# Optimization experiments

Measured on AMD Instinct MI355X. Metric: run time of the kernel, lower is better.

Reference implementation:

```python
import jax, jax.numpy as jnp
import numpy as np
from jax import lax

B, S, H = 4, 2048, 2048
E, TOPK = 32, 8
I_MOE = 768
I_SHARED = 4096


def setup_inputs() -> dict:
    key = jax.random.key(0)
    ks = jax.random.split(key, 9)
    sc = 0.02
    return {
        "hidden_states": jax.random.normal(ks[0], (B, S, H), jnp.float32),
        "gate_w": jax.random.normal(ks[1], (H, E), jnp.float32) * sc,
        "Wg": jax.random.normal(ks[2], (E, H, I_MOE), jnp.float32) * sc,
        "Wu": jax.random.normal(ks[3], (E, H, I_MOE), jnp.float32) * sc,
        "Wd": jax.random.normal(ks[4], (E, I_MOE, H), jnp.float32) * sc,
        "Sg": jax.random.normal(ks[5], (H, I_SHARED), jnp.float32) * sc,
        "Su": jax.random.normal(ks[6], (H, I_SHARED), jnp.float32) * sc,
        "Sd": jax.random.normal(ks[7], (I_SHARED, H), jnp.float32) * sc,
        "shared_gate_w": jax.random.normal(ks[8], (H, 1), jnp.float32) * sc,
    }


def reference(hidden_states, gate_w, Wg, Wu, Wd, Sg, Su, Sd, shared_gate_w):
    b, s, h = hidden_states.shape
    x = hidden_states.reshape(-1, h)                      # [T, H]
    T = x.shape[0]

    # router: softmax in fp32, top-k, renormalize (norm_topk_prob=True)
    router_logits = x @ gate_w                            # [T, E]
    probs = jax.nn.softmax(router_logits.astype(jnp.float32), axis=-1)
    topk_w, topk_idx = lax.top_k(probs, TOPK)             # [T, K]
    topk_w = topk_w / jnp.sum(topk_w, axis=-1, keepdims=True)
    topk_w = topk_w.astype(x.dtype)

    # dense combine weights: zero for unrouted (token, expert) pairs
    combine = jnp.zeros((T, E), x.dtype).at[jnp.arange(T)[:, None], topk_idx].add(topk_w)

    # scan over experts: SwiGLU MLP, weighted accumulate (scatter-combine)
    def step(acc, packed):
        wg, wu, wd, cw = packed                           # cw: [T]
        hmid = jax.nn.silu(x @ wg) * (x @ wu)             # [T, I_MOE]
        return acc + (hmid @ wd) * cw[:, None], None

    moe_out, _ = lax.scan(step, jnp.zeros_like(x), (Wg, Wu, Wd, combine.T))

    # shared expert with sigmoid gate
    shared = (jax.nn.silu(x @ Sg) * (x @ Su)) @ Sd        # [T, H]
    shared = jax.nn.sigmoid(x @ shared_gate_w) * shared

    final = (moe_out + shared).reshape(b, s, h)
    return final, router_logits
```

## Files before the change

### kernel.cpp

```cpp
#include <hip/hip_runtime.h>
#include <stdint.h>

#define T_TOK 8192
#define HD    2048
#define NE    32
#define KTOP  8
#define IM    768
#define IS    4096

typedef unsigned short u16;
typedef __attribute__((ext_vector_type(8))) short bf16x8;
typedef __attribute__((ext_vector_type(4))) float f32x4;

__device__ __forceinline__ u16 f2b(float f) {
    union { float f; unsigned u; } c; c.f = f;
    unsigned u = c.u;
    return (u16)((u + 0x7FFFu + ((u >> 16) & 1u)) >> 16);
}

__device__ __forceinline__ void gld16(const void* g, void* l) {
    __builtin_amdgcn_global_load_lds(
        (__attribute__((address_space(1))) void*)(uintptr_t)g,
        (__attribute__((address_space(3))) void*)(uint32_t)(uintptr_t)l,
        16, 0, 0);
}

__global__ __launch_bounds__(256) void router_kernel(
    const float* __restrict__ x, const float* __restrict__ gate_w,
    const float* __restrict__ sgw, float* __restrict__ logits_out,
    u16* __restrict__ xb, float* __restrict__ sgvals,
    int* __restrict__ topk_idx, float* __restrict__ topk_w,
    int* __restrict__ counts)
{
    const int t = blockIdx.x, tid = threadIdx.x;
    __shared__ __align__(16) float xrow[HD];
    __shared__ float red[256];
    __shared__ float sh_logit[NE];

    const float4* xr = (const float4*)(x + (size_t)t * HD);
    float4 v0 = xr[tid * 2], v1 = xr[tid * 2 + 1];
    *(float4*)&xrow[tid * 8]     = v0;
    *(float4*)&xrow[tid * 8 + 4] = v1;
    ushort4 p0; p0.x = f2b(v0.x); p0.y = f2b(v0.y); p0.z = f2b(v0.z); p0.w = f2b(v0.w);
    ushort4 p1; p1.x = f2b(v1.x); p1.y = f2b(v1.y); p1.z = f2b(v1.z); p1.w = f2b(v1.w);
    *(ushort4*)&xb[(size_t)t * HD + tid * 8]     = p0;
    *(ushort4*)&xb[(size_t)t * HD + tid * 8 + 4] = p1;
    __syncthreads();

    const int e = tid & 31, seg = tid >> 5;
    float acc = 0.f;
    const float* gwp = gate_w + e;
    for (int j = seg * 256; j < seg * 256 + 256; ++j)
        acc = fmaf(xrow[j], gwp[j * NE], acc);
    red[tid] = acc;
    __syncthreads();
    if (tid < NE) {
        float l = 0.f;
        #pragma unroll
        for (int s = 0; s < 8; ++s) l += red[s * 32 + tid];
        sh_logit[tid] = l;
        logits_out[(size_t)t * NE + tid] = l;
    }
    __syncthreads();

    float sacc = v0.x * sgw[tid * 8 + 0] + v0.y * sgw[tid * 8 + 1] + v0.z * sgw[tid * 8 + 2] + v0.w * sgw[tid * 8 + 3]
               + v1.x * sgw[tid * 8 + 4] + v1.y * sgw[tid * 8 + 5] + v1.z * sgw[tid * 8 + 6] + v1.w * sgw[tid * 8 + 7];
    red[tid] = sacc;
    __syncthreads();
    if (tid < 128) red[tid] += red[tid + 128];
    __syncthreads();
    if (tid < 64) {
        float s2 = red[tid] + red[tid + 64];
        #pragma unroll
        for (int off = 32; off; off >>= 1) s2 += __shfl_xor(s2, off, 64);
        if (tid == 0) sgvals[t] = 1.f / (1.f + __expf(-s2));

        float v = (tid < NE) ? sh_logit[tid] : -3.0e38f;
        float m = v;
        #pragma unroll
        for (int off = 32; off; off >>= 1) m = fmaxf(m, __shfl_xor(m, off, 64));
        float p = __expf(v - m);
        if (tid >= NE) p = 0.f;
        float ssum = p;
        #pragma unroll
        for (int off = 32; off; off >>= 1) ssum += __shfl_xor(ssum, off, 64);
        float myp = p / ssum;

        float selv[KTOP]; int seli[KTOP];
        float sumtop = 0.f;
        #pragma unroll
        for (int k = 0; k < KTOP; ++k) {
            float bv = myp; int bi = tid;
            #pragma unroll
            for (int off = 32; off; off >>= 1) {
                float ov = __shfl_xor(bv, off, 64);
                int   oi = __shfl_xor(bi, off, 64);
                if (ov > bv || (ov == bv && oi < bi)) { bv = ov; bi = oi; }
            }
            selv[k] = bv; seli[k] = bi; sumtop += bv;
            if (tid == bi) myp = -1.f;
        }
        if (tid == 0) {
            #pragma unroll
            for (int k = 0; k < KTOP; ++k) {
                topk_idx[(size_t)t * KTOP + k] = seli[k];
                topk_w[(size_t)t * KTOP + k]   = selv[k] / sumtop;
                atomicAdd(&counts[seli[k]], 1);
            }
        }
    }
}

__global__ void offsets_kernel(const int* __restrict__ counts,
                               int* __restrict__ offsets, int* __restrict__ cursor)
{
    if (threadIdx.x == 0) {
        int a = 0;
        for (int e = 0; e < NE; ++e) { offsets[e] = a; cursor[e] = a; a += counts[e]; }
    }
}

__global__ __launch_bounds__(256) void scatter_kernel(
    const int* __restrict__ topk_idx, const float* __restrict__ topk_w,
    int* __restrict__ cursor, int* __restrict__ token_list, float* __restrict__ weight_list)
{
    int i = blockIdx.x * 256 + threadIdx.x;
    int e = topk_idx[i];
    int pos = atomicAdd(&cursor[e], 1);
    token_list[pos]  = i >> 3;
    weight_list[pos] = topk_w[i];
}

__global__ __launch_bounds__(256) void convert_k(
    const float* __restrict__ W, u16* __restrict__ P, int K, int N)
{
    const int n0 = blockIdx.x * 128, kt = blockIdx.y * 32;
    const size_t eoff = (size_t)blockIdx.z * K * N;
    const int tid = threadIdx.x;
    __shared__ __align__(16) float tile[32][128];

    const float* Wb = W + eoff + (size_t)kt * N + n0;
    #pragma unroll
    for (int p = 0; p < 4; ++p) {
        int k = p * 8 + (tid >> 5);
        *(float4*)&tile[k][(tid & 31) * 4] = *(const float4*)(Wb + (size_t)k * N + (tid & 31) * 4);
    }
    __syncthreads();

    const int kblk = K >> 5;
    u16* Pp = P + eoff + ((size_t)blockIdx.x * kblk + blockIdx.y) * 4096;
    #pragma unroll
    for (int s = 0; s < 2; ++s) {
        int i = s * 256 + tid;
        int c = i >> 7, n = i & 127;
        union { u16 us[8]; uint4 v; } pk;
        #pragma unroll
        for (int q = 0; q < 8; ++q) pk.us[q] = f2b(tile[c * 8 + q][n]);
        *(uint4*)&Pp[(size_t)i * 8] = pk.v;
    }
}

template<int MODE>
__global__ __launch_bounds__(256, 2) void gemm_f(
    const u16* __restrict__ Asrc, const u16* __restrict__ B0p,
    const u16* __restrict__ B1p, u16* __restrict__ outb,
    float* __restrict__ outf, const float* __restrict__ scale,
    const int* __restrict__ token_list, const int* __restrict__ counts,
    const int* __restrict__ offsets)
{
    constexpr bool DUAL   = (MODE == 0 || MODE == 2);
    constexpr bool EXPERT = (MODE >= 2);
    constexpr int KTOT = (MODE == 0 || MODE == 2) ? HD : (MODE == 1 ? IS : IM);
    constexpr int NTOT = (MODE == 0) ? IS : (MODE == 2 ? IM : HD);
    constexpr int NTIL = DUAL ? 3 : 2;
    constexpr int NKT  = KTOT / 32;

    const int tid = threadIdx.x;
    const int ex  = blockIdx.z;
    const int n_e = EXPERT ? counts[ex]  : T_TOK;
    const int off = EXPERT ? offsets[ex] : 0;
    const int m0  = blockIdx.y * 128;
    if (m0 >= n_e) return;
    const int n0 = blockIdx.x * 128;

    const size_t ewoff = EXPERT ? (size_t)ex * KTOT * NTOT : 0;

    __shared__ __align__(16) u16 sh[2 * NTIL * 4096];

    const int w = tid >> 6, lane = tid & 63;
    const int lr = lane & 15, quad = lane >> 4;
    const int wm = (w >> 1) * 64, wn = (w & 1) * 64;
    const int ldsw = w * 512;

    const u16* asrc[2];
    #pragma unroll
    for (int s = 0; s < 2; ++s) {
        int i = s * 256 + tid;
        int c = i >> 7, r = i & 127;
        int grow = m0 + r;
        int gc = grow < n_e ? grow : n_e - 1;
        size_t rowidx;
        if (MODE == 0 || MODE == 1) rowidx = (size_t)grow;
        else if (MODE == 2) rowidx = (size_t)token_list[off + gc];
        else rowidx = (size_t)(off + gc);
        asrc[s] = Asrc + rowidx * KTOT + c * 8;
    }
    const u16* b0 = B0p + ewoff + ((size_t)(n0 >> 7) * NKT) * 4096 + (size_t)tid * 8;
    const u16* b1 = nullptr;
    if constexpr (DUAL) b1 = B1p + ewoff + ((size_t)(n0 >> 7) * NKT) * 4096 + (size_t)tid * 8;

    auto stage = [&](int buf, int kt) {
        u16* A  = sh + (size_t)(buf * NTIL + 0) * 4096;
        u16* Bt = sh + (size_t)(buf * NTIL + 1) * 4096;
        #pragma unroll
        for (int s = 0; s < 2; ++s) {
            gld16(asrc[s] + kt, A + s * 2048 + ldsw);
            gld16(b0 + (size_t)(kt >> 5) * 4096 + s * 2048, Bt + s * 2048 + ldsw);
        }
        if constexpr (DUAL) {
            u16* Bu = sh + (size_t)(buf * NTIL + 2) * 4096;
            #pragma unroll
            for (int s = 0; s < 2; ++s)
                gld16(b1 + (size_t)(kt >> 5) * 4096 + s * 2048, Bu + s * 2048 + ldsw);
        }
    };

    f32x4 acc0[4][4], acc1[4][4];
    #pragma unroll
    for (int a = 0; a < 4; ++a)
        #pragma unroll
        for (int b = 0; b < 4; ++b)
            #pragma unroll
            for (int q = 0; q < 4; ++q) { acc0[a][b][q] = 0.f; if constexpr (DUAL) acc1[a][b][q] = 0.f; }

    stage(0, 0);
    int cur = 0;
    for (int kt = 0; kt < KTOT; kt += 32) {
        __syncthreads();
        if (kt + 32 < KTOT) stage(cur ^ 1, kt + 32);

        const u16* A  = sh + (size_t)(cur * NTIL + 0) * 4096;
        const u16* B0 = sh + (size_t)(cur * NTIL + 1) * 4096;

        bf16x8 af[4], bf0[4], bf1[4];
        #pragma unroll
        for (int mt = 0; mt < 4; ++mt)
            af[mt]  = *(const bf16x8*)&A [quad * 1024 + (wm + mt * 16 + lr) * 8];
        #pragma unroll
        for (int nt = 0; nt < 4; ++nt)
            bf0[nt] = *(const bf16x8*)&B0[quad * 1024 + (wn + nt * 16 + lr) * 8];
        if constexpr (DUAL) {
            const u16* B1 = sh + (size_t)(cur * NTIL + 2) * 4096;
            #pragma unroll
            for (int nt = 0; nt < 4; ++nt)
                bf1[nt] = *(const bf16x8*)&B1[quad * 1024 + (wn + nt * 16 + lr) * 8];
        }
        #pragma unroll
        for (int mt = 0; mt < 4; ++mt)
            #pragma unroll
            for (int nt = 0; nt < 4; ++nt) {
                acc0[mt][nt] = __builtin_amdgcn_mfma_f32_16x16x32_bf16(af[mt], bf0[nt], acc0[mt][nt], 0, 0, 0);
                if constexpr (DUAL)
                    acc1[mt][nt] = __builtin_amdgcn_mfma_f32_16x16x32_bf16(af[mt], bf1[nt], acc1[mt][nt], 0, 0, 0);
            }
        cur ^= 1;
    }

    if (MODE == 0 || MODE == 2) {
        #pragma unroll
        for (int mt = 0; mt < 4; ++mt)
            #pragma unroll
            for (int rg = 0; rg < 4; ++rg) {
                const int grow = m0 + wm + mt * 16 + quad * 4 + rg;
                if (!EXPERT || grow < n_e) {
                    u16* orow = outb + (size_t)(EXPERT ? (off + grow) : grow) * NTOT + n0 + wn + lr;
                    #pragma unroll
                    for (int nt = 0; nt < 4; ++nt) {
                        float g = acc0[mt][nt][rg];
                        float u = acc1[mt][nt][rg];
                        float sgm = 1.f / (1.f + __expf(-g));
                        orow[nt * 16] = f2b(g * sgm * u);
                    }
                }
            }
    } else if (MODE == 1) {
        #pragma unroll
        for (int mt = 0; mt < 4; ++mt)
            #pragma unroll
            for (int rg = 0; rg < 4; ++rg) {
                const int grow = m0 + wm + mt * 16 + quad * 4 + rg;
                const float s = scale[grow];
                float* orow = outf + (size_t)grow * HD + n0 + wn + lr;
                #pragma unroll
                for (int nt = 0; nt < 4; ++nt) orow[nt * 16] = s * acc0[mt][nt][rg];
            }
    } else {
        #pragma unroll
        for (int mt = 0; mt < 4; ++mt)
            #pragma unroll
            for (int rg = 0; rg < 4; ++rg) {
                const int grow = m0 + wm + mt * 16 + quad * 4 + rg;
                if (grow < n_e) {
                    const int tok   = token_list[off + grow];
                    const float wgt = scale[off + grow];
                    float* orow = outf + (size_t)tok * HD + n0 + wn + lr;
                    #pragma unroll
                    for (int nt = 0; nt < 4; ++nt)
                        unsafeAtomicAdd(&orow[nt * 16], wgt * acc0[mt][nt][rg]);
                }
            }
    }
}

template<int MODE>
__global__ __launch_bounds__(256, 2) void gemm_l(
    const u16* __restrict__ Asrc, const float* __restrict__ B0g,
    const float* __restrict__ B1g, u16* __restrict__ outb,
    float* __restrict__ outf, const float* __restrict__ scale,
    const int* __restrict__ token_list, const int* __restrict__ counts,
    const int* __restrict__ offsets)
{
    constexpr bool DUAL   = (MODE == 0 || MODE == 2);
    constexpr bool EXPERT = (MODE >= 2);
    constexpr int KTOT = (MODE == 0 || MODE == 2) ? HD : (MODE == 1 ? IS : IM);
    constexpr int NTOT = (MODE == 0) ? IS : (MODE == 2 ? IM : HD);
    constexpr int LDA  = (MODE == 0 || MODE == 2) ? HD : (MODE == 1 ? IS : IM);

    const int tid = threadIdx.x;
    const int ex  = blockIdx.z;
    const int n_e = EXPERT ? counts[ex]  : T_TOK;
    const int off = EXPERT ? offsets[ex] : 0;
    const int m0  = blockIdx.y * 128;
    if (m0 >= n_e) return;
    const int n0 = blockIdx.x * 128;

    const float* B0 = B0g + (EXPERT ? (size_t)ex * KTOT * NTOT : 0);
    const float* B1 = DUAL ? (B1g + (EXPERT ? (size_t)ex * KTOT * NTOT : 0)) : nullptr;

    __shared__ __align__(16) u16 As [128 * 40];
    __shared__ __align__(16) u16 Bs0[128 * 40];
    __shared__ __align__(16) u16 Bs1[DUAL ? 128 * 40 : 8];

    const u16* aptr[2]; int aoff[2];
    #pragma unroll
    for (int i = 0; i < 2; ++i) {
        int c = tid + i * 256;
        int r = c >> 2, xo = c & 3;
        int grow = m0 + r;
        size_t rowidx;
        if (MODE == 0 || MODE == 1) rowidx = (size_t)grow;
        else if (MODE == 2) rowidx = (size_t)((grow < n_e) ? token_list[off + grow] : 0);
        else rowidx = (size_t)(off + grow);
        aptr[i] = Asrc + rowidx * LDA + xo * 8;
        aoff[i] = r * 40 + xo * 8;
    }

    const int kb = tid >> 5, nb = tid & 31;
    const float* bp0 = B0 + (size_t)(kb * 4) * NTOT + n0 + nb * 4;
    const float* bp1 = DUAL ? (B1 + (size_t)(kb * 4) * NTOT + n0 + nb * 4) : nullptr;
    const int bo = (nb * 4) * 40 + kb * 4;

    const int lane = tid & 63, wv = tid >> 6;
    const int wm = (wv >> 1) * 64, wn = (wv & 1) * 64;
    const int lr = lane & 15, quad = lane >> 4;

    f32x4 acc0[4][4], acc1[4][4];
    #pragma unroll
    for (int a = 0; a < 4; ++a)
        #pragma unroll
        for (int b = 0; b < 4; ++b)
            #pragma unroll
            for (int q = 0; q < 4; ++q) { acc0[a][b][q] = 0.f; if (DUAL) acc1[a][b][q] = 0.f; }

    for (int kt = 0; kt < KTOT; kt += 32) {
        uint4 av0 = *(const uint4*)(aptr[0] + kt);
        uint4 av1 = *(const uint4*)(aptr[1] + kt);
        float4 b0v[4], b1v[4];
        #pragma unroll
        for (int i = 0; i < 4; ++i) b0v[i] = *(const float4*)(bp0 + (size_t)(kt + i) * NTOT);
        if (DUAL) {
            #pragma unroll
            for (int i = 0; i < 4; ++i) b1v[i] = *(const float4*)(bp1 + (size_t)(kt + i) * NTOT);
        }
        __syncthreads();
        *(uint4*)&As[aoff[0]] = av0;
        *(uint4*)&As[aoff[1]] = av1;
        {
            const float* f0 = (const float*)b0v;
            #pragma unroll
            for (int j = 0; j < 4; ++j) {
                ushort4 tw; tw.x = f2b(f0[0 * 4 + j]); tw.y = f2b(f0[1 * 4 + j]);
                            tw.z = f2b(f0[2 * 4 + j]); tw.w = f2b(f0[3 * 4 + j]);
                *(ushort4*)&Bs0[bo + j * 40] = tw;
            }
        }
        if (DUAL) {
            const float* f1 = (const float*)b1v;
            #pragma unroll
            for (int j = 0; j < 4; ++j) {
                ushort4 tw; tw.x = f2b(f1[0 * 4 + j]); tw.y = f2b(f1[1 * 4 + j]);
                            tw.z = f2b(f1[2 * 4 + j]); tw.w = f2b(f1[3 * 4 + j]);
                *(ushort4*)&Bs1[bo + j * 40] = tw;
            }
        }
        __syncthreads();

        bf16x8 af[4], bf0[4], bf1[4];
        #pragma unroll
        for (int mt = 0; mt < 4; ++mt) af[mt]  = *(const bf16x8*)&As [(wm + mt * 16 + lr) * 40 + quad * 8];
        #pragma unroll
        for (int nt = 0; nt < 4; ++nt) bf0[nt] = *(const bf16x8*)&Bs0[(wn + nt * 16 + lr) * 40 + quad * 8];
        if (DUAL) {
            #pragma unroll
            for (int nt = 0; nt < 4; ++nt) bf1[nt] = *(const bf16x8*)&Bs1[(wn + nt * 16 + lr) * 40 + quad * 8];
        }
        #pragma unroll
        for (int mt = 0; mt < 4; ++mt)
            #pragma unroll
            for (int nt = 0; nt < 4; ++nt) {
                acc0[mt][nt] = __builtin_amdgcn_mfma_f32_16x16x32_bf16(af[mt], bf0[nt], acc0[mt][nt], 0, 0, 0);
                if (DUAL)
                    acc1[mt][nt] = __builtin_amdgcn_mfma_f32_16x16x32_bf16(af[mt], bf1[nt], acc1[mt][nt], 0, 0, 0);
            }
    }

    if (MODE == 0 || MODE == 2) {
        #pragma unroll
        for (int mt = 0; mt < 4; ++mt)
            #pragma unroll
            for (int rg = 0; rg < 4; ++rg) {
                const int grow = m0 + wm + mt * 16 + quad * 4 + rg;
                if (!EXPERT || grow < n_e) {
                    u16* orow = outb + (size_t)(EXPERT ? (off + grow) : grow) * NTOT + n0 + wn + lr;
                    #pragma unroll
                    for (int nt = 0; nt < 4; ++nt) {
                        float g = acc0[mt][nt][rg];
                        float u = acc1[mt][nt][rg];
                        float sgm = 1.f / (1.f + __expf(-g));
                        orow[nt * 16] = f2b(g * sgm * u);
                    }
                }
            }
    } else if (MODE == 1) {
        #pragma unroll
        for (int mt = 0; mt < 4; ++mt)
            #pragma unroll
            for (int rg = 0; rg < 4; ++rg) {
                const int grow = m0 + wm + mt * 16 + quad * 4 + rg;
                const float s = scale[grow];
                float* orow = outf + (size_t)grow * HD + n0 + wn + lr;
                #pragma unroll
                for (int nt = 0; nt < 4; ++nt) orow[nt * 16] = s * acc0[mt][nt][rg];
            }
    } else {
        #pragma unroll
        for (int mt = 0; mt < 4; ++mt)
            #pragma unroll
            for (int rg = 0; rg < 4; ++rg) {
                const int grow = m0 + wm + mt * 16 + quad * 4 + rg;
                if (grow < n_e) {
                    const int tok   = token_list[off + grow];
                    const float wgt = scale[off + grow];
                    float* orow = outf + (size_t)tok * HD + n0 + wn + lr;
                    #pragma unroll
                    for (int nt = 0; nt < 4; ++nt)
                        unsafeAtomicAdd(&orow[nt * 16], wgt * acc0[mt][nt][rg]);
                }
            }
    }
}

#define OFF_XB      ((size_t)0)
#define OFF_HSH     ((size_t)33554432)
#define OFF_HMID    ((size_t)100663296)
#define OFF_SG      ((size_t)201326592)
#define OFF_TOPKI   ((size_t)201359360)
#define OFF_TOPKW   ((size_t)201621504)
#define OFF_TOKL    ((size_t)201883648)
#define OFF_WGTL    ((size_t)202145792)
#define OFF_COUNTS  ((size_t)202407936)
#define OFF_CURSOR  ((size_t)202408064)
#define OFF_OFFSETS ((size_t)202408192)
#define OFF_PWG     ((size_t)202408448)
#define OFF_PWU     ((size_t)303071744)
#define OFF_PWD     ((size_t)403735040)
#define OFF_PSG     ((size_t)504398336)
#define OFF_PSU     ((size_t)521175552)
#define OFF_PSD     ((size_t)537952768)
#define WS_NEED     ((size_t)554729984)

extern "C" void kernel_launch(void* const* d_in, const int* in_sizes, int n_in,
                              void* d_out, int out_size, void* d_ws, size_t ws_size,
                              hipStream_t stream)
{
    const float* x   = (const float*)d_in[0];
    const float* gw  = (const float*)d_in[1];
    const float* Wg  = (const float*)d_in[2];
    const float* Wu  = (const float*)d_in[3];
    const float* Wd  = (const float*)d_in[4];
    const float* Sg  = (const float*)d_in[5];
    const float* Su  = (const float*)d_in[6];
    const float* Sd  = (const float*)d_in[7];
    const float* sgw = (const float*)d_in[8];

    float* out        = (float*)d_out;
    float* logits_out = out + (size_t)T_TOK * HD;

    char* ws = (char*)d_ws;
    u16*   xb      = (u16*)  (ws + OFF_XB);
    u16*   hshared = (u16*)  (ws + OFF_HSH);
    u16*   hmid    = (u16*)  (ws + OFF_HMID);
    float* sgvals  = (float*)(ws + OFF_SG);
    int*   topk_i  = (int*)  (ws + OFF_TOPKI);
    float* topk_wv = (float*)(ws + OFF_TOPKW);
    int*   tok_lst = (int*)  (ws + OFF_TOKL);
    float* wgt_lst = (float*)(ws + OFF_WGTL);
    int*   counts  = (int*)  (ws + OFF_COUNTS);
    int*   cursor  = (int*)  (ws + OFF_CURSOR);
    int*   offsets = (int*)  (ws + OFF_OFFSETS);

    hipMemsetAsync(counts, 0, 256, stream);

    router_kernel<<<T_TOK, 256, 0, stream>>>(x, gw, sgw, logits_out, xb, sgvals,
                                             topk_i, topk_wv, counts);
    offsets_kernel<<<1, 64, 0, stream>>>(counts, offsets, cursor);
    scatter_kernel<<<T_TOK * KTOP / 256, 256, 0, stream>>>(topk_i, topk_wv, cursor,
                                                           tok_lst, wgt_lst);

    if (ws_size >= WS_NEED) {
        u16* pWg = (u16*)(ws + OFF_PWG);
        u16* pWu = (u16*)(ws + OFF_PWU);
        u16* pWd = (u16*)(ws + OFF_PWD);
        u16* pSg = (u16*)(ws + OFF_PSG);
        u16* pSu = (u16*)(ws + OFF_PSU);
        u16* pSd = (u16*)(ws + OFF_PSD);

        convert_k<<<dim3(IM / 128, HD / 32, NE), 256, 0, stream>>>(Wg, pWg, HD, IM);
        convert_k<<<dim3(IM / 128, HD / 32, NE), 256, 0, stream>>>(Wu, pWu, HD, IM);
        convert_k<<<dim3(HD / 128, IM / 32, NE), 256, 0, stream>>>(Wd, pWd, IM, HD);
        convert_k<<<dim3(IS / 128, HD / 32, 1),  256, 0, stream>>>(Sg, pSg, HD, IS);
        convert_k<<<dim3(IS / 128, HD / 32, 1),  256, 0, stream>>>(Su, pSu, HD, IS);
        convert_k<<<dim3(HD / 128, IS / 32, 1),  256, 0, stream>>>(Sd, pSd, IS, HD);

        gemm_f<0><<<dim3(IS / 128, T_TOK / 128, 1), 256, 0, stream>>>(
            xb, pSg, pSu, hshared, nullptr, nullptr, nullptr, nullptr, nullptr);
        gemm_f<2><<<dim3(IM / 128, T_TOK / 128, NE), 256, 0, stream>>>(
            xb, pWg, pWu, hmid, nullptr, nullptr, tok_lst, counts, offsets);
        gemm_f<1><<<dim3(HD / 128, T_TOK / 128, 1), 256, 0, stream>>>(
            hshared, pSd, nullptr, nullptr, out, sgvals, nullptr, nullptr, nullptr);
        gemm_f<3><<<dim3(HD / 128, T_TOK / 128, NE), 256, 0, stream>>>(
            hmid, pWd, nullptr, nullptr, out, wgt_lst, tok_lst, counts, offsets);
    } else {
        gemm_l<0><<<dim3(IS / 128, T_TOK / 128, 1), 256, 0, stream>>>(
            xb, Sg, Su, hshared, nullptr, nullptr, nullptr, nullptr, nullptr);
        gemm_l<2><<<dim3(IM / 128, T_TOK / 128, NE), 256, 0, stream>>>(
            xb, Wg, Wu, hmid, nullptr, nullptr, tok_lst, counts, offsets);
        gemm_l<1><<<dim3(HD / 128, T_TOK / 128, 1), 256, 0, stream>>>(
            hshared, Sd, nullptr, nullptr, out, sgvals, nullptr, nullptr, nullptr);
        gemm_l<3><<<dim3(HD / 128, T_TOK / 128, NE), 256, 0, stream>>>(
            hmid, Wd, nullptr, nullptr, out, wgt_lst, tok_lst, counts, offsets);
    }
}
```

Measured before the change: 2.830 ms.

## Triple-buffer GEMM LDS pipeline with vmcnt waits, XCD swizzle, and MFMA priority

Moves the GEMM main loop from double-buffered LDS staging with a full __syncthreads to a three-stage ring that prefetches two k-tiles ahead. Waits use explicit s_waitcnt vmcnt counts plus a raw barrier, so one tile's loads stay in flight while the current tile computes. Also remaps block indices so neighbouring tiles land on the same XCD for L2 reuse, raises wave priority around the MFMA block, and raises the occupancy hint for the single-B modes. In exchange it uses more LDS per block, which can lower occupancy, and the hand-counted vmcnt values must match the number of loads stage() issues.

```diff
diff --git a/kernel.cpp b/kernel.cpp
--- a/kernel.cpp
+++ b/kernel.cpp
@@ -23,6 +23,14 @@
         (__attribute__((address_space(1))) void*)(uintptr_t)g,
         (__attribute__((address_space(3))) void*)(uint32_t)(uintptr_t)l,
         16, 0, 0);
+}
+
+__device__ __forceinline__ void xcd_swizzle(int& bx, int& by, int& bz) {
+    const int gx = gridDim.x, gy = gridDim.y, gz = gridDim.z;
+    const int nwg = gx * gy * gz;
+    int f = blockIdx.x + gx * (blockIdx.y + gy * blockIdx.z);
+    if ((nwg & 7) == 0) f = (f & 7) * (nwg >> 3) + (f >> 3);
+    bx = f % gx; f /= gx; by = f % gy; bz = f / gy;
 }
 
 __global__ __launch_bounds__(256) void router_kernel(
@@ -161,7 +169,7 @@
 }
 
 template<int MODE>
-__global__ __launch_bounds__(256, 2) void gemm_f(
+__global__ __launch_bounds__(256, (MODE == 0 || MODE == 2) ? 2 : 3) void gemm_f(
     const u16* __restrict__ Asrc, const u16* __restrict__ B0p,
     const u16* __restrict__ B1p, u16* __restrict__ outb,
     float* __restrict__ outf, const float* __restrict__ scale,
@@ -176,16 +184,18 @@
     constexpr int NKT  = KTOT / 32;
 
     const int tid = threadIdx.x;
-    const int ex  = blockIdx.z;
+    int bx, by, bz;
+    xcd_swizzle(bx, by, bz);
+    const int ex  = bz;
     const int n_e = EXPERT ? counts[ex]  : T_TOK;
     const int off = EXPERT ? offsets[ex] : 0;
-    const int m0  = blockIdx.y * 128;
+    const int m0  = by * 128;
     if (m0 >= n_e) return;
-    const int n0 = blockIdx.x * 128;
+    const int n0 = bx * 128;
 
     const size_t ewoff = EXPERT ? (size_t)ex * KTOT * NTOT : 0;
 
-    __shared__ __align__(16) u16 sh[2 * NTIL * 4096];
+    __shared__ __align__(16) u16 sh[3 * NTIL * 4096];
 
     const int w = tid >> 6, lane = tid & 63;
     const int lr = lane & 15, quad = lane >> 4;
@@ -234,10 +244,16 @@
             for (int q = 0; q < 4; ++q) { acc0[a][b][q] = 0.f; if constexpr (DUAL) acc1[a][b][q] = 0.f; }
 
     stage(0, 0);
+    stage(1, 32);
+    if constexpr (DUAL) asm volatile("s_waitcnt vmcnt(6)" ::: "memory");
+    else                asm volatile("s_waitcnt vmcnt(4)" ::: "memory");
+    __builtin_amdgcn_s_barrier();
+    __builtin_amdgcn_sched_barrier(0);
+
     int cur = 0;
     for (int kt = 0; kt < KTOT; kt += 32) {
-        __syncthreads();
-        if (kt + 32 < KTOT) stage(cur ^ 1, kt + 32);
+        const bool issued = (kt + 64 < KTOT);
+        if (issued) stage(cur == 0 ? 2 : cur - 1, kt + 64);
 
         const u16* A  = sh + (size_t)(cur * NTIL + 0) * 4096;
         const u16* B0 = sh + (size_t)(cur * NTIL + 1) * 4096;
@@ -255,6 +271,7 @@
             for (int nt = 0; nt < 4; ++nt)
                 bf1[nt] = *(const bf16x8*)&B1[quad * 1024 + (wn + nt * 16 + lr) * 8];
         }
+        __builtin_amdgcn_s_setprio(1);
         #pragma unroll
         for (int mt = 0; mt < 4; ++mt)
             #pragma unroll
@@ -263,7 +280,19 @@
                 if constexpr (DUAL)
                     acc1[mt][nt] = __builtin_amdgcn_mfma_f32_16x16x32_bf16(af[mt], bf1[nt], acc1[mt][nt], 0, 0, 0);
             }
-        cur ^= 1;
+        __builtin_amdgcn_s_setprio(0);
+
+        if (kt + 32 < KTOT) {
+            if (issued) {
+                if constexpr (DUAL) asm volatile("s_waitcnt vmcnt(6)" ::: "memory");
+                else                asm volatile("s_waitcnt vmcnt(4)" ::: "memory");
+            } else {
+                asm volatile("s_waitcnt vmcnt(0)" ::: "memory");
+            }
+            __builtin_amdgcn_s_barrier();
+            __builtin_amdgcn_sched_barrier(0);
+        }
+        cur = (cur == 2) ? 0 : cur + 1;
     }
 
     if (MODE == 0 || MODE == 2) {
```

Result: no change. 2.808 ms (-0.8%).
